# Kernel optimization log

Measured on AMD Instinct MI355X. Metric: run time of the kernel, lower is better.

## Reference

```python
import jax, jax.numpy as jnp
import numpy as np
from jax import lax

SIGMA = 1.0          # block_elemnts.combined_sigma
BN_EPS = 1e-5


def setup_inputs() -> dict:
    key = jax.random.key(0)
    k1, k2, k3, k4 = jax.random.split(key, 4)
    B, N, T, C_in, C_out = 8, 1024, 8, 64, 64
    return {
        "points": jax.random.normal(k1, (B, N, 3), dtype=jnp.float32),
        "translations": jax.random.normal(k2, (B, T, 3), dtype=jnp.float32),
        "functions": jax.random.normal(k3, (B, N, C_in), dtype=jnp.float32),
        "k_tensor": jax.random.normal(k4, (C_out, C_in, T), dtype=jnp.float32)
            * np.sqrt(2.0 / (C_in + C_out)),  # xavier_normal_
        "gamma": jnp.ones((C_out,), dtype=jnp.float32),
        "beta": jnp.zeros((C_out,), dtype=jnp.float32),
    }


def reference(points, translations, functions, k_tensor, gamma, beta):
    denom = 2.0 * SIGMA ** 2
    # pairwise squared distances [B,N,N]
    sq = jnp.sum(points * points, axis=-1)                      # [B,N]
    dist = sq[:, :, None] + sq[:, None, :] \
        - 2.0 * jnp.einsum('bnd,bmd->bnm', points, points)      # [B,N,N]
    # interpolation matrix = Gaussian kernel of distances
    interp_rowsum = jnp.sum(jnp.exp(-dist / denom), axis=2, keepdims=True)  # [B,N,1]
    w = functions / interp_rowsum                               # [B,N,Cin]
    # b_tensor[t] = w @ k_tensor[:,:,t]^T  -> [T,B,N,Cout]
    b = jnp.einsum('bnc,oct->tbno', w, k_tensor)
    ptd = jnp.einsum('bnd,btd->tbn', points, translations)      # [T,B,N]
    tsq = jnp.sum(translations * translations, axis=2).T        # [T,B]

    B_, N_, O_ = b.shape[1], b.shape[2], b.shape[3]

    def step(acc, inputs):
        b_t, ptd_t, tsq_t = inputs                              # [B,N,O],[B,N],[B]
        dot = -2.0 * ptd_t                                      # [B,N]
        # exponent = -||p_i - p_j - t||^2 / (2*sigma^2), always <= 0
        q = jnp.exp(-(dist + dot[:, :, None] - dot[:, None, :]
                      + tsq_t[:, None, None]) / denom)          # [B,N,N]
        return acc + jnp.einsum('bnm,bmo->bno', q, b_t), None

    out, _ = lax.scan(step, jnp.zeros((B_, N_, O_), dtype=b.dtype),
                      (b, ptd, tsq))                            # [B,N,O]

    # BatchNorm1d in training mode over (B,N) per channel, then ReLU
    mean = jnp.mean(out, axis=(0, 1))
    var = jnp.var(out, axis=(0, 1))
    xn = (out - mean) * lax.rsqrt(var + BN_EPS) * gamma + beta
    return jax.nn.relu(xn)                                      # [B,N,Cout]
```

## Files before the change

kernel.cpp:

```cpp
#include <hip/hip_runtime.h>
#include <hip/hip_bf16.h>
#include <cstdint>
#include <cstddef>

#define BN_EPS 1e-5f

typedef float f32x4_t __attribute__((ext_vector_type(4)));
typedef __bf16 bf16x8_t __attribute__((ext_vector_type(8)));

__device__ __forceinline__ unsigned short f2bf(float f) {
    __hip_bfloat16 h = __float2bfloat16(f);
    return __builtin_bit_cast(unsigned short, h);
}
__device__ __forceinline__ float bf2f(unsigned short u) {
    unsigned int v = ((unsigned int)u) << 16;
    return __builtin_bit_cast(float, v);
}

__device__ __forceinline__ void gld_lds16(void* lds, const void* gp) {
#if __has_builtin(__builtin_amdgcn_global_load_lds)
    __builtin_amdgcn_global_load_lds(
        (const __attribute__((address_space(1))) unsigned int*)gp,
        (__attribute__((address_space(3))) unsigned int*)lds, 16, 0, 0);
#else
    *(uint4*)lds = *(const uint4*)gp;
#endif
}


__global__ __launch_bounds__(256) void k_g(const float* __restrict__ points,
                                           const float* __restrict__ ktens,
                                           float* __restrict__ rowsum,
                                           unsigned short* __restrict__ kpb,
                                           float* __restrict__ bns) {
    __shared__ float praw[3072];
    __shared__ float px[1024], py[1024], pz[1024], hq[1024];
    __shared__ float part[8][128];
    __shared__ float p2[8][32];

    const int tid = threadIdx.x;
    if (blockIdx.x >= 1024) {
        const int i = (blockIdx.x - 1024) * 256 + tid;
        const int t = i >> 12, o = (i >> 6) & 63, c = i & 63;
        kpb[i] = f2bf(ktens[(o * 64 + c) * 8 + t]);
        if (blockIdx.x == 1024 && tid < 128) bns[tid] = 0.f;
        return;
    }

    const int b  = blockIdx.x & 7;
    const int n0 = (blockIdx.x >> 3) * 8;

    for (int i = tid; i < 3072; i += 256) praw[i] = points[b * 3072 + i];
    __syncthreads();
    for (int n = tid; n < 1024; n += 256) {
        float x = praw[n * 3], y = praw[n * 3 + 1], z = praw[n * 3 + 2];
        px[n] = x; py[n] = y; pz[n] = z;
        hq[n] = -0.5f * (x * x + y * y + z * z);
    }
    __syncthreads();

    const int rhalf = tid >> 7;
    const int c0 = (tid & 127) * 8;
    float vx[8], vy[8], vz[8], vh[8];
    *(float4*)&vx[0] = *(const float4*)&px[c0];
    *(float4*)&vx[4] = *(const float4*)&px[c0 + 4];
    *(float4*)&vy[0] = *(const float4*)&py[c0];
    *(float4*)&vy[4] = *(const float4*)&py[c0 + 4];
    *(float4*)&vz[0] = *(const float4*)&pz[c0];
    *(float4*)&vz[4] = *(const float4*)&pz[c0 + 4];
    *(float4*)&vh[0] = *(const float4*)&hq[c0];
    *(float4*)&vh[4] = *(const float4*)&hq[c0 + 4];

    #pragma unroll
    for (int u = 0; u < 4; ++u) {
        const int rl = u * 2 + rhalf;
        const int row = n0 + rl;
        const float rx = px[row], ry = py[row], rz = pz[row], hr = hq[row];
        float ssum = 0.f;
        #pragma unroll
        for (int j = 0; j < 8; ++j)
            ssum += __expf(hr + vh[j] + rx * vx[j] + ry * vy[j] + rz * vz[j]);
        part[rl][tid & 127] = ssum;
    }
    __syncthreads();
    {
        const int row = tid >> 5, c4l = (tid & 31) * 4;
        float4 p = *(const float4*)&part[row][c4l];
        p2[row][tid & 31] = p.x + p.y + p.z + p.w;
    }
    __syncthreads();
    if (tid < 8) {
        float s = 0.f;
        #pragma unroll
        for (int q = 0; q < 8; ++q) {
            float4 v = *(const float4*)&p2[tid][q * 4];
            s += v.x + v.y + v.z + v.w;
        }
        rowsum[b * 1024 + n0 + tid] = s;
    }
}

__global__ __launch_bounds__(256) void k_prep(const float* __restrict__ points,
                                              const float* __restrict__ trans,
                                              const float* __restrict__ funcs,
                                              const unsigned short* __restrict__ kpb,
                                              const float* __restrict__ rowsum,
                                              unsigned short* __restrict__ bmatT,
                                              float* __restrict__ escale) {
    __shared__ unsigned short Asm[128 * 72];
    __shared__ unsigned short Bsm[128 * 72];
    __shared__ float sfacl[256];

    const int b  = blockIdx.x & 7;
    const int mt = (blockIdx.x >> 3) & 7;
    const int ct = blockIdx.x >> 6;
    const int m0 = mt * 128;

    const int tid  = threadIdx.x;
    const int wave = tid >> 6, lane = tid & 63;
    const int wr = wave >> 1, wc = wave & 1;
    const int fr = lane & 15, quad = lane >> 4;

    {
        const int tloc = tid >> 7, m = tid & 127;
        const int t = ct * 2 + tloc;
        const float tx = trans[b * 24 + t * 3], ty = trans[b * 24 + t * 3 + 1],
                    tz = trans[b * 24 + t * 3 + 2];
        const float* pp = &points[(size_t)(b * 1024 + m0 + m) * 3];
        const float ptd = pp[0] * tx + pp[1] * ty + pp[2] * tz;
        const float tsq = tx * tx + ty * ty + tz * tz;
        const float rsv = rowsum[b * 1024 + m0 + m];
        sfacl[tloc * 128 + m] = __expf(-ptd - 0.5f * tsq) / rsv;
        escale[(size_t)(b * 8 + t) * 1024 + m0 + m] = __expf(ptd);
    }
    #pragma unroll
    for (int rep = 0; rep < 2; ++rep) {
        const int m = rep * 64 + (tid >> 2);
        const int c16 = (tid & 3) * 16;
        const float* fp = &funcs[((size_t)(b * 1024) + m0 + m) * 64 + c16];
        float4 f0 = *(const float4*)fp, f1 = *(const float4*)(fp + 4);
        float4 f2 = *(const float4*)(fp + 8), f3 = *(const float4*)(fp + 12);
        uint4 p0, p1;
        p0.x = f2bf(f0.x) | ((unsigned)f2bf(f0.y) << 16);
        p0.y = f2bf(f0.z) | ((unsigned)f2bf(f0.w) << 16);
        p0.z = f2bf(f1.x) | ((unsigned)f2bf(f1.y) << 16);
        p0.w = f2bf(f1.z) | ((unsigned)f2bf(f1.w) << 16);
        p1.x = f2bf(f2.x) | ((unsigned)f2bf(f2.y) << 16);
        p1.y = f2bf(f2.z) | ((unsigned)f2bf(f2.w) << 16);
        p1.z = f2bf(f3.x) | ((unsigned)f2bf(f3.y) << 16);
        p1.w = f2bf(f3.z) | ((unsigned)f2bf(f3.w) << 16);
        *(uint4*)&Asm[m * 72 + c16] = p0;
        *(uint4*)&Asm[m * 72 + c16 + 8] = p1;
    }
    #pragma unroll
    for (int rep = 0; rep < 4; ++rep) {
        const int col = rep * 32 + (tid >> 3);
        const int c8 = (tid & 7) * 8;
        uint4 v = *(const uint4*)&kpb[(size_t)(ct * 128 + col) * 64 + c8];
        *(uint4*)&Bsm[col * 72 + c8] = v;
    }
    __syncthreads();

    f32x4_t acc[4][4];
    #pragma unroll
    for (int i = 0; i < 4; ++i)
        #pragma unroll
        for (int j = 0; j < 4; ++j) acc[i][j] = f32x4_t{0.f, 0.f, 0.f, 0.f};

    #pragma unroll
    for (int s = 0; s < 2; ++s) {
        uint4 afr[4], bfr[4];
        #pragma unroll
        for (int i = 0; i < 4; ++i)
            afr[i] = *(const uint4*)&Asm[(wr * 64 + i * 16 + fr) * 72 + s * 32 + quad * 8];
        #pragma unroll
        for (int j = 0; j < 4; ++j)
            bfr[j] = *(const uint4*)&Bsm[(wc * 64 + j * 16 + fr) * 72 + s * 32 + quad * 8];
        #pragma unroll
        for (int i = 0; i < 4; ++i)
            #pragma unroll
            for (int j = 0; j < 4; ++j)
                acc[i][j] = __builtin_amdgcn_mfma_f32_16x16x32_bf16(
                    __builtin_bit_cast(bf16x8_t, afr[i]),
                    __builtin_bit_cast(bf16x8_t, bfr[j]),
                    acc[i][j], 0, 0, 0);
    }

    #pragma unroll
    for (int i = 0; i < 4; ++i) {
        #pragma unroll
        for (int j = 0; j < 4; ++j) {
            const int colg = ct * 128 + wc * 64 + j * 16 + fr;
            ushort4 pk;
            {
                const int mb = wr * 64 + i * 16 + quad * 4;
                pk.x = f2bf(acc[i][j][0] * sfacl[wc * 128 + mb + 0]);
                pk.y = f2bf(acc[i][j][1] * sfacl[wc * 128 + mb + 1]);
                pk.z = f2bf(acc[i][j][2] * sfacl[wc * 128 + mb + 2]);
                pk.w = f2bf(acc[i][j][3] * sfacl[wc * 128 + mb + 3]);
                *(ushort4*)&bmatT[(size_t)(b * 512 + colg) * 1024 + m0 + mb] = pk;
            }
        }
    }
}

__global__ __launch_bounds__(256, 2) void k_gemm(const float* __restrict__ points,
                                                 const unsigned short* __restrict__ bmatT,
                                                 const float* __restrict__ escale,
                                                 unsigned short* __restrict__ He2) {
    __shared__ unsigned short Bs[8192];
    __shared__ float escT[1024];
    __shared__ float4 mp[256];

    const int b  = blockIdx.x & 7;
    const int rt = (blockIdx.x >> 3) & 7;
    const int z  = blockIdx.x >> 6;
    const int ogp = z & 1;
    const int kh  = z >> 1;
    const int n0 = rt * 128;
    const int kb = kh * 256;

    const int tid  = threadIdx.x;
    const int wave = tid >> 6, lane = tid & 63;

    {
        const int t = tid >> 5, r4 = (tid & 31) * 4;
        *(float4*)&escT[t * 128 + r4] =
            *(const float4*)&escale[(size_t)(b * 8 + t) * 1024 + n0 + r4];
    }
    {
        const float* pp = &points[(size_t)(b * 1024 + kb + tid) * 3];
        const float x = pp[0], y = pp[1], zz = pp[2];
        mp[tid] = make_float4(x, y, zz, -0.5f * (x * x + y * y + zz * zz));
    }

    const unsigned short* gB = bmatT + (size_t)(b * 512 + ogp * 32) * 1024 + kb;

    const int r16 = lane >> 2;
    const int kq  = lane & 3;
    const int gsw = kq ^ (r16 & 3);

    const int fr = lane & 15;
    const int quad = lane >> 4;
    const int swoff = (quad ^ (fr & 3)) << 4;
    const int row_base = wave * 32;

    float rx0, ry0, rz0, rh0, rx1, ry1, rz1, rh1;
    {
        const float* p0 = &points[(size_t)(b * 1024 + n0 + row_base + fr) * 3];
        rx0 = p0[0]; ry0 = p0[1]; rz0 = p0[2];
        rh0 = -0.5f * (rx0 * rx0 + ry0 * ry0 + rz0 * rz0);
        const float* p1 = &points[(size_t)(b * 1024 + n0 + row_base + 16 + fr) * 3];
        rx1 = p1[0]; ry1 = p1[1]; rz1 = p1[2];
        rh1 = -0.5f * (rx1 * rx1 + ry1 * ry1 + rz1 * rz1);
    }

    f32x4_t acc[2][16];
    #pragma unroll
    for (int i = 0; i < 2; ++i)
        #pragma unroll
        for (int j = 0; j < 16; ++j) acc[i][j] = f32x4_t{0.f, 0.f, 0.f, 0.f};

    for (int kk = 0; kk < 8; ++kk) {
        const int k0 = kk * 32;
        __syncthreads();
        #pragma unroll
        for (int i = 0; i < 4; ++i) {
            const int seg = wave * 4 + i;
            const int t = seg >> 1, oh = (seg & 1) * 16;
            gld_lds16((char*)Bs + seg * 1024 + lane * 16,
                      gB + (size_t)(t * 64 + oh + r16) * 1024 + k0 + gsw * 8);
        }
        uint4 afr0, afr1;
        {
            unsigned short u0[8], u1[8];
            const int mbase = k0 + quad * 8;
            #pragma unroll
            for (int j = 0; j < 8; ++j) {
                const float4 m4 = mp[mbase + j];
                const float e0 = __expf(rh0 + m4.w + rx0 * m4.x + ry0 * m4.y + rz0 * m4.z);
                const float e1 = __expf(rh1 + m4.w + rx1 * m4.x + ry1 * m4.y + rz1 * m4.z);
                u0[j] = f2bf(e0);
                u1[j] = f2bf(e1);
            }
            afr0.x = u0[0] | ((unsigned)u0[1] << 16);
            afr0.y = u0[2] | ((unsigned)u0[3] << 16);
            afr0.z = u0[4] | ((unsigned)u0[5] << 16);
            afr0.w = u0[6] | ((unsigned)u0[7] << 16);
            afr1.x = u1[0] | ((unsigned)u1[1] << 16);
            afr1.y = u1[2] | ((unsigned)u1[3] << 16);
            afr1.z = u1[4] | ((unsigned)u1[5] << 16);
            afr1.w = u1[6] | ((unsigned)u1[7] << 16);
        }
        __syncthreads();
        #pragma unroll
        for (int j = 0; j < 16; ++j) {
            uint4 bfr = *(const uint4*)((const char*)Bs + (j * 16 + fr) * 64 + swoff);
            acc[0][j] = __builtin_amdgcn_mfma_f32_16x16x32_bf16(
                __builtin_bit_cast(bf16x8_t, afr0),
                __builtin_bit_cast(bf16x8_t, bfr), acc[0][j], 0, 0, 0);
            acc[1][j] = __builtin_amdgcn_mfma_f32_16x16x32_bf16(
                __builtin_bit_cast(bf16x8_t, afr1),
                __builtin_bit_cast(bf16x8_t, bfr), acc[1][j], 0, 0, 0);
        }
    }

    const int oo = lane & 15;
    unsigned short* dst = He2 + (size_t)kh * 524288
                              + (size_t)(b * 1024 + n0) * 64 + ogp * 32;
    #pragma unroll
    for (int i = 0; i < 2; ++i) {
        #pragma unroll
        for (int r = 0; r < 4; ++r) {
            const int row = row_base + i * 16 + quad * 4 + r;
            float s0 = 0.f, s1 = 0.f;
            #pragma unroll
            for (int t = 0; t < 8; ++t) {
                const float e = escT[t * 128 + row];
                s0 += e * acc[i][2 * t][r];
                s1 += e * acc[i][2 * t + 1][r];
            }
            dst[(size_t)row * 64 + oo] = f2bf(s0);
            dst[(size_t)row * 64 + 16 + oo] = f2bf(s1);
        }
    }
}

__global__ __launch_bounds__(256) void k_fin(const unsigned short* __restrict__ He2,
                                             float* __restrict__ out,
                                             float* __restrict__ bns) {
    __shared__ float s1[16][64], s2[16][64];
    const int tid = threadIdx.x;
    float a0 = 0.f, a1 = 0.f, a2 = 0.f, a3 = 0.f;
    float q0 = 0.f, q1 = 0.f, q2 = 0.f, q3 = 0.f;
    #pragma unroll
    for (int it = 0; it < 2; ++it) {
        const size_t idx = (size_t)blockIdx.x * 512 + it * 256 + tid;
        float4 s = make_float4(0.f, 0.f, 0.f, 0.f);
        #pragma unroll
        for (int p = 0; p < 4; ++p) {
            ushort4 u = *(const ushort4*)(He2 + (size_t)p * 524288 + idx * 4);
            s.x += bf2f(u.x); s.y += bf2f(u.y); s.z += bf2f(u.z); s.w += bf2f(u.w);
        }
        ((float4*)out)[idx] = s;
        a0 += s.x; a1 += s.y; a2 += s.z; a3 += s.w;
        q0 += s.x * s.x; q1 += s.y * s.y; q2 += s.z * s.z; q3 += s.w * s.w;
    }
    const int g = tid >> 4, o4 = (tid & 15) * 4;
    *(float4*)&s1[g][o4] = make_float4(a0, a1, a2, a3);
    *(float4*)&s2[g][o4] = make_float4(q0, q1, q2, q3);
    __syncthreads();
    if (tid < 64) {
        float sa = 0.f, sb = 0.f;
        #pragma unroll
        for (int r = 0; r < 16; ++r) { sa += s1[r][tid]; sb += s2[r][tid]; }
        atomicAdd(&bns[tid], sa);
        atomicAdd(&bns[64 + tid], sb);
    }
}

__global__ __launch_bounds__(256) void k_bn(float* __restrict__ out,
                                            const float* __restrict__ bns,
                                            const float* __restrict__ gamma,
                                            const float* __restrict__ beta) {
    const int i = blockIdx.x * 256 + threadIdx.x;
    const int o4 = (i & 15) * 4;
    float4 x = ((float4*)out)[i];
    const float4 s  = *(const float4*)&bns[o4];
    const float4 s2 = *(const float4*)&bns[64 + o4];
    const float4 gm = *(const float4*)&gamma[o4];
    const float4 bt = *(const float4*)&beta[o4];
    const float invn = 1.f / 8192.f;
    float m, v, w;
    m = s.x * invn; v = s2.x * invn - m * m; w = __frsqrt_rn(v + BN_EPS) * gm.x;
    x.x = fmaxf((x.x - m) * w + bt.x, 0.f);
    m = s.y * invn; v = s2.y * invn - m * m; w = __frsqrt_rn(v + BN_EPS) * gm.y;
    x.y = fmaxf((x.y - m) * w + bt.y, 0.f);
    m = s.z * invn; v = s2.z * invn - m * m; w = __frsqrt_rn(v + BN_EPS) * gm.z;
    x.z = fmaxf((x.z - m) * w + bt.z, 0.f);
    m = s.w * invn; v = s2.w * invn - m * m; w = __frsqrt_rn(v + BN_EPS) * gm.w;
    x.w = fmaxf((x.w - m) * w + bt.w, 0.f);
    ((float4*)out)[i] = x;
}

extern "C" void kernel_launch(void* const* d_in, const int* in_sizes, int n_in,
                              void* d_out, int out_size, void* d_ws, size_t ws_size,
                              hipStream_t stream) {
    const float* points = (const float*)d_in[0];
    const float* trans  = (const float*)d_in[1];
    const float* funcs  = (const float*)d_in[2];
    const float* ktens  = (const float*)d_in[3];
    const float* gamma  = (const float*)d_in[4];
    const float* beta   = (const float*)d_in[5];
    float* out = (float*)d_out;

    float* ws      = (float*)d_ws;
    float* escale  = ws;
    float* bns     = escale + 65536;
    float* rowsum  = bns + 128;
    unsigned short* He2   = (unsigned short*)(rowsum + 8192);
    unsigned short* kpb   = He2 + 2097152;
    unsigned short* bmatT = kpb + 32768;

    k_g<<<1152, 256, 0, stream>>>(points, ktens, rowsum, kpb, bns);
    k_prep<<<256, 256, 0, stream>>>(points, trans, funcs, kpb, rowsum, bmatT, escale);
    k_gemm<<<512, 256, 0, stream>>>(points, bmatT, escale, He2);
    k_fin<<<256, 256, 0, stream>>>(He2, out, bns);
    k_bn<<<512, 256, 0, stream>>>(out, bns, gamma, beta);
}
```

Before: 106.2 us.

## Double-buffer GEMM B tiles, widen rowsum blocks, remap finalize block order

The main GEMM kernel now double-buffers its B tile in LDS. It prefetches the next k-slice through async global-to-LDS loads while computing the current one, and uses explicit vmcnt waits and barriers in place of two __syncthreads per iteration. The rowsum kernel handles 16 rows per block instead of 8, which halves the block count and the redundant per-block point staging. The finalize and BN kernels swizzle their block indices, likely to spread memory traffic across channels. The changes double the LDS use in the GEMM, which may hurt its 2-blocks-per-CU occupancy, and the hand-written waitcnt logic is fragile.

```diff
diff --git a/kernel.cpp b/kernel.cpp
--- a/kernel.cpp
+++ b/kernel.cpp
@@ -35,20 +35,20 @@
                                            float* __restrict__ bns) {
     __shared__ float praw[3072];
     __shared__ float px[1024], py[1024], pz[1024], hq[1024];
-    __shared__ float part[8][128];
-    __shared__ float p2[8][32];
+    __shared__ float part[16][128];
+    __shared__ float p2[16][32];
 
     const int tid = threadIdx.x;
-    if (blockIdx.x >= 1024) {
-        const int i = (blockIdx.x - 1024) * 256 + tid;
+    if (blockIdx.x >= 512) {
+        const int i = (blockIdx.x - 512) * 256 + tid;
         const int t = i >> 12, o = (i >> 6) & 63, c = i & 63;
         kpb[i] = f2bf(ktens[(o * 64 + c) * 8 + t]);
-        if (blockIdx.x == 1024 && tid < 128) bns[tid] = 0.f;
+        if (blockIdx.x == 512 && tid < 128) bns[tid] = 0.f;
         return;
     }
 
     const int b  = blockIdx.x & 7;
-    const int n0 = (blockIdx.x >> 3) * 8;
+    const int n0 = (blockIdx.x >> 3) * 16;
 
     for (int i = tid; i < 3072; i += 256) praw[i] = points[b * 3072 + i];
     __syncthreads();
@@ -72,7 +72,7 @@
     *(float4*)&vh[4] = *(const float4*)&hq[c0 + 4];
 
     #pragma unroll
-    for (int u = 0; u < 4; ++u) {
+    for (int u = 0; u < 8; ++u) {
         const int rl = u * 2 + rhalf;
         const int row = n0 + rl;
         const float rx = px[row], ry = py[row], rz = pz[row], hr = hq[row];
@@ -83,13 +83,14 @@
         part[rl][tid & 127] = ssum;
     }
     __syncthreads();
-    {
-        const int row = tid >> 5, c4l = (tid & 31) * 4;
+    #pragma unroll
+    for (int rep = 0; rep < 2; ++rep) {
+        const int row = rep * 8 + (tid >> 5), c4l = (tid & 31) * 4;
         float4 p = *(const float4*)&part[row][c4l];
         p2[row][tid & 31] = p.x + p.y + p.z + p.w;
     }
     __syncthreads();
-    if (tid < 8) {
+    if (tid < 16) {
         float s = 0.f;
         #pragma unroll
         for (int q = 0; q < 8; ++q) {
@@ -208,7 +209,7 @@
                                                  const unsigned short* __restrict__ bmatT,
                                                  const float* __restrict__ escale,
                                                  unsigned short* __restrict__ He2) {
-    __shared__ unsigned short Bs[8192];
+    __shared__ unsigned short Bs[2][8192];
     __shared__ float escT[1024];
     __shared__ float4 mp[256];
 
@@ -222,17 +223,6 @@
 
     const int tid  = threadIdx.x;
     const int wave = tid >> 6, lane = tid & 63;
-
-    {
-        const int t = tid >> 5, r4 = (tid & 31) * 4;
-        *(float4*)&escT[t * 128 + r4] =
-            *(const float4*)&escale[(size_t)(b * 8 + t) * 1024 + n0 + r4];
-    }
-    {
-        const float* pp = &points[(size_t)(b * 1024 + kb + tid) * 3];
-        const float x = pp[0], y = pp[1], zz = pp[2];
-        mp[tid] = make_float4(x, y, zz, -0.5f * (x * x + y * y + zz * zz));
-    }
 
     const unsigned short* gB = bmatT + (size_t)(b * 512 + ogp * 32) * 1024 + kb;
 
@@ -254,6 +244,24 @@
         rx1 = p1[0]; ry1 = p1[1]; rz1 = p1[2];
         rh1 = -0.5f * (rx1 * rx1 + ry1 * ry1 + rz1 * rz1);
     }
+    {
+        const int t = tid >> 5, r4 = (tid & 31) * 4;
+        float4 ev = *(const float4*)&escale[(size_t)(b * 8 + t) * 1024 + n0 + r4];
+        const float* pp = &points[(size_t)(b * 1024 + kb + tid) * 3];
+        const float x = pp[0], y = pp[1], zz = pp[2];
+        *(float4*)&escT[t * 128 + r4] = ev;
+        mp[tid] = make_float4(x, y, zz, -0.5f * (x * x + y * y + zz * zz));
+    }
+    __builtin_amdgcn_sched_barrier(0);
+    #pragma unroll
+    for (int i = 0; i < 4; ++i) {
+        const int seg = wave * 4 + i;
+        const int tt = seg >> 1, oh = (seg & 1) * 16;
+        gld_lds16((char*)Bs[0] + seg * 1024 + lane * 16,
+                  gB + (size_t)(tt * 64 + oh + r16) * 1024 + gsw * 8);
+    }
+    asm volatile("s_waitcnt lgkmcnt(0)" ::: "memory");
+    __builtin_amdgcn_s_barrier();
 
     f32x4_t acc[2][16];
     #pragma unroll
@@ -262,19 +270,21 @@
         for (int j = 0; j < 16; ++j) acc[i][j] = f32x4_t{0.f, 0.f, 0.f, 0.f};
 
     for (int kk = 0; kk < 8; ++kk) {
-        const int k0 = kk * 32;
-        __syncthreads();
-        #pragma unroll
-        for (int i = 0; i < 4; ++i) {
-            const int seg = wave * 4 + i;
-            const int t = seg >> 1, oh = (seg & 1) * 16;
-            gld_lds16((char*)Bs + seg * 1024 + lane * 16,
-                      gB + (size_t)(t * 64 + oh + r16) * 1024 + k0 + gsw * 8);
+        const int cur = kk & 1;
+        if (kk < 7) {
+            const int k0n = (kk + 1) * 32;
+            #pragma unroll
+            for (int i = 0; i < 4; ++i) {
+                const int seg = wave * 4 + i;
+                const int tt = seg >> 1, oh = (seg & 1) * 16;
+                gld_lds16((char*)Bs[cur ^ 1] + seg * 1024 + lane * 16,
+                          gB + (size_t)(tt * 64 + oh + r16) * 1024 + k0n + gsw * 8);
+            }
         }
         uint4 afr0, afr1;
         {
             unsigned short u0[8], u1[8];
-            const int mbase = k0 + quad * 8;
+            const int mbase = kk * 32 + quad * 8;
             #pragma unroll
             for (int j = 0; j < 8; ++j) {
                 const float4 m4 = mp[mbase + j];
@@ -292,10 +302,13 @@
             afr1.z = u1[4] | ((unsigned)u1[5] << 16);
             afr1.w = u1[6] | ((unsigned)u1[7] << 16);
         }
-        __syncthreads();
+        if (kk < 7) asm volatile("s_waitcnt vmcnt(4)" ::: "memory");
+        else        asm volatile("s_waitcnt vmcnt(0)" ::: "memory");
+        __builtin_amdgcn_s_barrier();
+        __builtin_amdgcn_sched_barrier(0);
         #pragma unroll
         for (int j = 0; j < 16; ++j) {
-            uint4 bfr = *(const uint4*)((const char*)Bs + (j * 16 + fr) * 64 + swoff);
+            uint4 bfr = *(const uint4*)((const char*)Bs[cur] + (j * 16 + fr) * 64 + swoff);
             acc[0][j] = __builtin_amdgcn_mfma_f32_16x16x32_bf16(
                 __builtin_bit_cast(bf16x8_t, afr0),
                 __builtin_bit_cast(bf16x8_t, bfr), acc[0][j], 0, 0, 0);
@@ -303,6 +316,7 @@
                 __builtin_bit_cast(bf16x8_t, afr1),
                 __builtin_bit_cast(bf16x8_t, bfr), acc[1][j], 0, 0, 0);
         }
+        if (kk < 7) __builtin_amdgcn_s_barrier();
     }
 
     const int oo = lane & 15;
@@ -331,11 +345,12 @@
                                              float* __restrict__ bns) {
     __shared__ float s1[16][64], s2[16][64];
     const int tid = threadIdx.x;
+    const int vb = ((blockIdx.x & 7) << 5) | (blockIdx.x >> 3);
     float a0 = 0.f, a1 = 0.f, a2 = 0.f, a3 = 0.f;
     float q0 = 0.f, q1 = 0.f, q2 = 0.f, q3 = 0.f;
     #pragma unroll
     for (int it = 0; it < 2; ++it) {
-        const size_t idx = (size_t)blockIdx.x * 512 + it * 256 + tid;
+        const size_t idx = (size_t)vb * 512 + it * 256 + tid;
         float4 s = make_float4(0.f, 0.f, 0.f, 0.f);
         #pragma unroll
         for (int p = 0; p < 4; ++p) {
@@ -363,7 +378,8 @@
                                             const float* __restrict__ bns,
                                             const float* __restrict__ gamma,
                                             const float* __restrict__ beta) {
-    const int i = blockIdx.x * 256 + threadIdx.x;
+    const int vb = ((blockIdx.x & 7) << 6) | (blockIdx.x >> 3);
+    const int i = vb * 256 + threadIdx.x;
     const int o4 = (i & 15) * 4;
     float4 x = ((float4*)out)[i];
     const float4 s  = *(const float4*)&bns[o4];
@@ -402,7 +418,7 @@
     unsigned short* kpb   = He2 + 2097152;
     unsigned short* bmatT = kpb + 32768;
 
-    k_g<<<1152, 256, 0, stream>>>(points, ktens, rowsum, kpb, bns);
+    k_g<<<640, 256, 0, stream>>>(points, ktens, rowsum, kpb, bns);
     k_prep<<<256, 256, 0, stream>>>(points, trans, funcs, kpb, rowsum, bmatT, escale);
     k_gemm<<<512, 256, 0, stream>>>(points, bmatT, escale, He2);
     k_fin<<<256, 256, 0, stream>>>(He2, out, bns);
```

Result: no change. 107.2 us (+1.0%).
